# Kernel tuning notes

Measured on AMD Instinct MI355X. Metric: run time of the kernel, lower is better.

Reference implementation:

```python
import jax, jax.numpy as jnp
import numpy as np

B, L, C = 8, 8192, 256
FOCAL_LEVEL = 3
KERNELS = [3, 5, 7]  # focal_factor*k + focal_x[0]
LN_EPS = 1e-3  # keras LayerNormalization default epsilon


def _gelu(x):
    return jax.nn.gelu(x, approximate=False)  # keras 'gelu' is exact


def _layernorm(x, g, b):
    m = jnp.mean(x, axis=-1, keepdims=True)
    v = jnp.var(x, axis=-1, keepdims=True)
    return (x - m) * jax.lax.rsqrt(v + LN_EPS) * g + b


def _conv1d_same(x, w, b):
    # x: [B,L,Cin], w: [K,Cin,Cout]
    y = jax.lax.conv_general_dilated(x, w, window_strides=(1,), padding='SAME',
                                     dimension_numbers=('NWC', 'WIO', 'NWC'))
    return y + b


def setup_inputs() -> dict:
    key = jax.random.key(0)
    ks = jax.random.split(key, 16)
    s = 0.02
    inp = {
        'x': jax.random.normal(ks[0], (B, L, C), dtype=jnp.float32),
        'f_w': jax.random.normal(ks[1], (C, 2 * C + FOCAL_LEVEL + 1), dtype=jnp.float32) * s,
        'f_b': jnp.zeros((2 * C + FOCAL_LEVEL + 1,), dtype=jnp.float32),
        'h_w': jax.random.normal(ks[2], (1, C, C), dtype=jnp.float32) * s,
        'h_b': jnp.zeros((C,), dtype=jnp.float32),
        'proj_w': jax.random.normal(ks[3], (C, C), dtype=jnp.float32) * s,
        'proj_b': jnp.zeros((C,), dtype=jnp.float32),
    }
    for l, K in enumerate(KERNELS):
        inp[f'conv_w{l}'] = jax.random.normal(ks[4 + l], (K, C, C), dtype=jnp.float32) * s
        inp[f'conv_b{l}'] = jnp.zeros((C,), dtype=jnp.float32)
        inp[f'ln_g{l}'] = jnp.ones((C,), dtype=jnp.float32)
        inp[f'ln_b{l}'] = jnp.zeros((C,), dtype=jnp.float32)
    return inp


def reference(x, f_w, f_b,
              conv_w0, conv_b0, ln_g0, ln_b0,
              conv_w1, conv_b1, ln_g1, ln_b1,
              conv_w2, conv_b2, ln_g2, ln_b2,
              h_w, h_b, proj_w, proj_b):
    x_fea = x @ f_w + f_b                      # [B,L,2C+4]
    q = x_fea[..., :C]
    ctx = x_fea[..., C:2 * C]
    gates = x_fea[..., 2 * C:]                 # [B,L,4]

    levels = [(conv_w0, conv_b0, ln_g0, ln_b0),
              (conv_w1, conv_b1, ln_g1, ln_b1),
              (conv_w2, conv_b2, ln_g2, ln_b2)]

    ctx_all = jnp.zeros_like(ctx)
    for l, (cw, cb, lg, lb) in enumerate(levels):
        ctx = _layernorm(_gelu(_conv1d_same(ctx, cw, cb)), lg, lb)
        ctx_all = ctx_all + ctx * gates[..., l:l + 1]

    # global average pool gate (broadcasts over L)
    ctx_global = jnp.mean(ctx, axis=1, keepdims=True) * gates[..., FOCAL_LEVEL:]
    ctx_all = ctx_all + ctx_global

    # h: 1x1 conv == dense
    ctx_all = jnp.einsum('blc,cd->bld', ctx_all, h_w[0]) + h_b
    x_out = (q * ctx_all) @ proj_w + proj_b    # proj_drop is identity at inference
    return x_out
```

## Files before the change

kernel.cpp:

```cpp
#include <hip/hip_runtime.h>
#include <math.h>

#define CDIM 256
#define LSEQ 8192
#define BATCH 8
#define MTOT (BATCH * LSEQ)
#define PADROWS 8208
#define PAD0 8

typedef unsigned short ushort_t;
typedef unsigned int uint_t;

typedef __bf16 bf16x8 __attribute__((ext_vector_type(8)));
typedef float f32x4 __attribute__((ext_vector_type(4)));

__device__ __forceinline__ ushort_t f2bf(float f) {
    union { float f; uint_t u; } v; v.f = f;
    uint_t u = v.u;
    return (ushort_t)((u + 0x7FFFu + ((u >> 16) & 1u)) >> 16);
}
__device__ __forceinline__ float bf2f(ushort_t h) {
    union { uint_t u; float f; } v; v.u = ((uint_t)h) << 16;
    return v.f;
}
__device__ __forceinline__ float gelu_exact(float x) {
    return 0.5f * x * (1.0f + erff(x * 0.70710678118654752440f));
}

__device__ __forceinline__ void gload16(const ushort_t* g, ushort_t* lds) {
    __builtin_amdgcn_global_load_lds(
        reinterpret_cast<__attribute__((address_space(1))) uint_t*>(
            reinterpret_cast<uintptr_t>(g)),
        reinterpret_cast<__attribute__((address_space(3))) uint_t*>(
            reinterpret_cast<uintptr_t>(lds)),
        16, 0, 0);
}

__global__ __launch_bounds__(256) void cvt_f32_bf16(const float* __restrict__ in,
                                                    ushort_t* __restrict__ out) {
    int i = blockIdx.x * 256 + threadIdx.x;
    float4 v = ((const float4*)in)[i];
    ushort4 o = { f2bf(v.x), f2bf(v.y), f2bf(v.z), f2bf(v.w) };
    ((ushort4*)out)[i] = o;
}

__global__ __launch_bounds__(256) void transpose_cvt(const float* __restrict__ in,
                                                     ushort_t* __restrict__ out,
                                                     int K, int N, int ldin, int col0) {
    __shared__ float t[32][33];
    int k0 = blockIdx.x * 32, n0 = blockIdx.y * 32;
    int tx = threadIdx.x, ty = threadIdx.y;
    #pragma unroll
    for (int i = 0; i < 4; i++) {
        int k = k0 + ty + i * 8;
        t[ty + i * 8][tx] = in[(size_t)k * ldin + col0 + n0 + tx];
    }
    __syncthreads();
    #pragma unroll
    for (int i = 0; i < 4; i++) {
        int n = n0 + ty + i * 8;
        out[(size_t)n * K + k0 + tx] = f2bf(t[tx][ty + i * 8]);
    }
}

__global__ __launch_bounds__(256) void zero_guards(ushort_t* __restrict__ ctx_pad) {
    int i = blockIdx.x * 256 + threadIdx.x;
    int c = i & 255;
    int r = (i >> 8) & 15;
    int b = i >> 12;
    int row = b * PADROWS + ((r < 8) ? r : (PADROWS - 16 + r));
    ctx_pad[(size_t)row * CDIM + c] = 0;
}

template <int MODE>
__global__ __launch_bounds__(256) void gemm_bf16(
    const ushort_t* __restrict__ A, const ushort_t* __restrict__ BT,
    const float* __restrict__ bias,
    float* __restrict__ C, ushort_t* __restrict__ q_out, ushort_t* __restrict__ ctx_pad,
    int Ktot)
{
    __shared__ __align__(16) ushort_t As[128 * 32];
    __shared__ __align__(16) ushort_t Bs[128 * 32];
    int tid = threadIdx.x;
    int w = tid >> 6, l = tid & 63;
    int bn = blockIdx.x * 128;
    int by = blockIdx.y;
    long arow0 = (long)by * 128;
    int crow0 = by * 128;

    int wr = w >> 1, wc = w & 1;
    int lr = l & 15, lk = (l >> 4) * 8;
    int sr = l >> 2;
    int sc = (l & 3) * 8;

    f32x4 acc[4][4] = {};

    int nsteps = Ktot >> 5;
    for (int kt = 0; kt < nsteps; ++kt) {
        int k0 = kt << 5;
        #pragma unroll
        for (int jj = 0; jj < 2; ++jj) {
            int j = w * 2 + jj;
            int r = j * 16 + sr;
            gload16(A + (arow0 + r) * CDIM + (k0 + sc), &As[j * 512]);
            gload16(BT + (long)(bn + r) * Ktot + (k0 + sc), &Bs[j * 512]);
        }
        __syncthreads();
        bf16x8 av[4], bv[4];
        #pragma unroll
        for (int m = 0; m < 4; ++m)
            av[m] = *reinterpret_cast<const bf16x8*>(&As[(wr * 64 + m * 16 + lr) * 32 + lk]);
        #pragma unroll
        for (int n = 0; n < 4; ++n)
            bv[n] = *reinterpret_cast<const bf16x8*>(&Bs[(wc * 64 + n * 16 + lr) * 32 + lk]);
        #pragma unroll
        for (int m = 0; m < 4; ++m)
            #pragma unroll
            for (int n = 0; n < 4; ++n)
                acc[m][n] = __builtin_amdgcn_mfma_f32_16x16x32_bf16(av[m], bv[n], acc[m][n], 0, 0, 0);
        __syncthreads();
    }

    int rbase = (l >> 4) * 4;
    #pragma unroll
    for (int n = 0; n < 4; ++n) {
        int col = bn + wc * 64 + n * 16 + lr;
        float bia = bias[col];
        #pragma unroll
        for (int m = 0; m < 4; ++m) {
            int rowb = crow0 + wr * 64 + m * 16 + rbase;
            #pragma unroll
            for (int r = 0; r < 4; ++r) {
                float v = acc[m][n][r] + bia;
                int row = rowb + r;
                if (MODE == 0) {
                    C[(size_t)row * CDIM + col] = v;
                } else if (MODE == 1) {
                    if (col < CDIM) {
                        q_out[(size_t)row * CDIM + col] = f2bf(v);
                    } else {
                        int bb = row >> 13, tb = row & (LSEQ - 1);
                        ctx_pad[((size_t)bb * PADROWS + PAD0 + tb) * CDIM + (col - CDIM)] = f2bf(v);
                    }
                } else {
                    size_t idx = (size_t)row * CDIM + col;
                    q_out[idx] = f2bf(bf2f(q_out[idx]) * v);
                }
            }
        }
    }
}

__device__ __forceinline__ void stageA_chunk(const ushort_t* Arow0, int cc,
                                             ushort_t* asb, int tid, int w) {
    int o = tid;
    int row = o >> 2, cp = o & 3;
    int cg = cp ^ (row & 3);
    gload16(Arow0 + (size_t)row * CDIM + cc * 32 + cg * 8, asb + (size_t)(w * 64) * 8);
    if (tid < 64) {
        int o2 = 512 + tid;
        int row2 = o2 >> 2, cp2 = o2 & 3;
        int cg2 = cp2 ^ (row2 & 3);
        gload16(Arow0 + (size_t)row2 * CDIM + cc * 32 + cg2 * 8, asb + (size_t)512 * 8);
    }
}
__device__ __forceinline__ void stageB_chunk(const ushort_t* BT, int Ktot, int koffB,
                                             ushort_t* bsb, int tid, int w) {
    #pragma unroll
    for (int i = 0; i < 2; ++i) {
        int o = tid + i * 512;
        int n = o >> 2, cp = o & 3;
        int cg = cp ^ ((n >> 1) & 3);
        gload16(BT + (size_t)n * Ktot + koffB + cg * 8, bsb + (size_t)(w * 64 + i * 512) * 8);
    }
}

__global__ __launch_bounds__(512, 4) void conv_fused(
    const ushort_t* __restrict__ A, const ushort_t* __restrict__ BT,
    const float* __restrict__ bias,
    const float* __restrict__ lng, const float* __restrict__ lnb,
    ushort_t* __restrict__ ctx_out, int KW, int Ktot)
{
    __shared__ __align__(16) ushort_t As2[2][144 * 32];
    __shared__ __align__(16) ushort_t Bs[2][256 * 32];

    int tid = threadIdx.x;
    int w = tid >> 6, l = tid & 63;
    int by = blockIdx.x;
    int b = by >> 6;
    int tloc = (by & 63) << 7;
    const ushort_t* Arow0 = A + ((size_t)b * PADROWS + PAD0 + tloc - 8) * CDIM;

    int wr = w >> 2;
    int wc = w & 3;
    int lr = l & 15;
    int quad = l >> 4;

    int P = KW >> 1;
    int hoff = 8 - P;
    f32x4 acc[4][4] = {};

    stageA_chunk(Arow0, 0, As2[0], tid, w);
    stageB_chunk(BT, Ktot, 0, Bs[0], tid, w);
    __syncthreads();

    int nIt = KW * 8;
    int it = 0;
    for (int c = 0; c < 8; ++c) {
        for (int tap = 0; tap < KW; ++tap, ++it) {
            if (tap == 0 && c < 7)
                stageA_chunk(Arow0, c + 1, As2[(c + 1) & 1], tid, w);
            if (it + 1 < nIt) {
                int tapn = tap + 1, cn = c;
                if (tapn == KW) { tapn = 0; cn = c + 1; }
                stageB_chunk(BT, Ktot, tapn * 256 + cn * 32, Bs[(it + 1) & 1], tid, w);
            }
            const ushort_t* asb = As2[c & 1];
            const ushort_t* bsb = Bs[it & 1];
            bf16x8 av[4], bv[4];
            #pragma unroll
            for (int m = 0; m < 4; ++m) {
                int row = wr * 64 + m * 16 + lr + tap + hoff;
                int cs = quad ^ (row & 3);
                av[m] = *reinterpret_cast<const bf16x8*>(&asb[row * 32 + cs * 8]);
            }
            #pragma unroll
            for (int n = 0; n < 4; ++n) {
                int nn = wc * 64 + n * 16 + lr;
                int cs = quad ^ ((nn >> 1) & 3);
                bv[n] = *reinterpret_cast<const bf16x8*>(&bsb[nn * 32 + cs * 8]);
            }
            #pragma unroll
            for (int m = 0; m < 4; ++m)
                #pragma unroll
                for (int n = 0; n < 4; ++n)
                    acc[m][n] = __builtin_amdgcn_mfma_f32_16x16x32_bf16(av[m], bv[n], acc[m][n], 0, 0, 0);
            __syncthreads();
        }
    }

    float* rs = (float*)&Bs[0][0];
    float* rq = rs + 512;
    float bias_c[4], lng_c[4], lnb_c[4];
    #pragma unroll
    for (int n = 0; n < 4; ++n) {
        int col = wc * 64 + n * 16 + lr;
        bias_c[n] = bias[col];
        lng_c[n] = lng[col];
        lnb_c[n] = lnb[col];
    }
    #pragma unroll
    for (int m = 0; m < 4; ++m) {
        #pragma unroll
        for (int r = 0; r < 4; ++r) {
            float s = 0.0f, sq = 0.0f;
            #pragma unroll
            for (int n = 0; n < 4; ++n) {
                float v = acc[m][n][r] + bias_c[n];
                v = gelu_exact(v);
                acc[m][n][r] = v;
                s += v; sq += v * v;
            }
            s += __shfl_xor(s, 1);  sq += __shfl_xor(sq, 1);
            s += __shfl_xor(s, 2);  sq += __shfl_xor(sq, 2);
            s += __shfl_xor(s, 4);  sq += __shfl_xor(sq, 4);
            s += __shfl_xor(s, 8);  sq += __shfl_xor(sq, 8);
            if (lr == 0) {
                int rl = wr * 64 + m * 16 + quad * 4 + r;
                rs[rl * 4 + wc] = s;
                rq[rl * 4 + wc] = sq;
            }
        }
    }
    __syncthreads();
    #pragma unroll
    for (int m = 0; m < 4; ++m) {
        #pragma unroll
        for (int r = 0; r < 4; ++r) {
            int rl = wr * 64 + m * 16 + quad * 4 + r;
            float mean = (rs[rl * 4] + rs[rl * 4 + 1] + rs[rl * 4 + 2] + rs[rl * 4 + 3]) * (1.0f / 256.0f);
            float var = (rq[rl * 4] + rq[rl * 4 + 1] + rq[rl * 4 + 2] + rq[rl * 4 + 3]) * (1.0f / 256.0f) - mean * mean;
            float inv = rsqrtf(var + 1e-3f);
            int trow = tloc + rl;
            ushort_t* cp = ctx_out + ((size_t)b * PADROWS + PAD0 + trow) * CDIM;
            #pragma unroll
            for (int n = 0; n < 4; ++n) {
                int col = wc * 64 + n * 16 + lr;
                float y = (acc[m][n][r] - mean) * inv * lng_c[n] + lnb_c[n];
                cp[col] = f2bf(y);
            }
        }
    }
}

__global__ __launch_bounds__(256) void gates_kernel(const float* __restrict__ x,
                                                    const float* __restrict__ f_w,
                                                    const float* __restrict__ f_b,
                                                    float* __restrict__ gates) {
    __shared__ float fcol[256][4];
    int tid = threadIdx.x;
    #pragma unroll
    for (int j = 0; j < 4; ++j) fcol[tid][j] = f_w[(size_t)tid * 516 + 512 + j];
    __syncthreads();
    int w = tid >> 6, l = tid & 63;
    int t = blockIdx.x * 4 + w;
    float4 xv = ((const float4*)(x + (size_t)t * CDIM))[l];
    int c = l * 4;
    float a[4];
    #pragma unroll
    for (int j = 0; j < 4; ++j)
        a[j] = xv.x * fcol[c][j] + xv.y * fcol[c + 1][j] + xv.z * fcol[c + 2][j] + xv.w * fcol[c + 3][j];
    #pragma unroll
    for (int off = 32; off >= 1; off >>= 1)
        #pragma unroll
        for (int j = 0; j < 4; ++j) a[j] += __shfl_xor(a[j], off);
    if (l == 0) {
        #pragma unroll
        for (int j = 0; j < 4; ++j) gates[(size_t)t * 4 + j] = a[j] + f_b[512 + j];
    }
}

__global__ __launch_bounds__(256) void col_mean_partial(const ushort_t* __restrict__ ctx_pad,
                                                        float* __restrict__ partial) {
    int b = blockIdx.x, chunk = blockIdx.y, c = threadIdx.x;
    const ushort_t* base = ctx_pad + ((size_t)b * PADROWS + PAD0 + chunk * 256) * CDIM + c;
    float s = 0.0f;
    for (int r = 0; r < 256; ++r) s += bf2f(base[(size_t)r * CDIM]);
    partial[((size_t)b * 32 + chunk) * CDIM + c] = s;
}

__global__ __launch_bounds__(256) void col_mean_final(const float* __restrict__ partial,
                                                      float* __restrict__ meanv) {
    int b = blockIdx.x, c = threadIdx.x;
    float s = 0.0f;
    for (int i = 0; i < 32; ++i) s += partial[((size_t)b * 32 + i) * CDIM + c];
    meanv[b * CDIM + c] = s * (1.0f / (float)LSEQ);
}

__global__ __launch_bounds__(256) void finalize_A(
    const ushort_t* __restrict__ c0buf, const ushort_t* __restrict__ c1buf,
    const ushort_t* __restrict__ c2buf,
    const float* __restrict__ meanv, const float* __restrict__ gates,
    ushort_t* __restrict__ A_bf)
{
    int i = blockIdx.x * 256 + threadIdx.x;
    int t = i >> 5;
    int c8 = (i & 31) * 8;
    int b = t >> 13, tb = t & (LSEQ - 1);
    size_t pidx = ((size_t)b * PADROWS + PAD0 + tb) * CDIM + c8;
    const float* g = gates + (size_t)t * 4;
    float g0 = g[0], g1 = g[1], g2 = g[2], g3 = g[3];
    ushort4 a0 = *(const ushort4*)(c0buf + pidx);
    ushort4 a1 = *(const ushort4*)(c0buf + pidx + 4);
    ushort4 b0 = *(const ushort4*)(c1buf + pidx);
    ushort4 b1 = *(const ushort4*)(c1buf + pidx + 4);
    ushort4 d0 = *(const ushort4*)(c2buf + pidx);
    ushort4 d1 = *(const ushort4*)(c2buf + pidx + 4);
    const float* mv = meanv + b * CDIM + c8;
    ushort_t out[8];
    ushort_t va[8] = { a0.x, a0.y, a0.z, a0.w, a1.x, a1.y, a1.z, a1.w };
    ushort_t vb[8] = { b0.x, b0.y, b0.z, b0.w, b1.x, b1.y, b1.z, b1.w };
    ushort_t vd[8] = { d0.x, d0.y, d0.z, d0.w, d1.x, d1.y, d1.z, d1.w };
    #pragma unroll
    for (int j = 0; j < 8; ++j) {
        float v = bf2f(va[j]) * g0 + bf2f(vb[j]) * g1 + bf2f(vd[j]) * g2 + mv[j] * g3;
        out[j] = f2bf(v);
    }
    *(ushort4*)(A_bf + (size_t)t * CDIM + c8)     = make_ushort4(out[0], out[1], out[2], out[3]);
    *(ushort4*)(A_bf + (size_t)t * CDIM + c8 + 4) = make_ushort4(out[4], out[5], out[6], out[7]);
}

extern "C" void kernel_launch(void* const* d_in, const int* in_sizes, int n_in,
                              void* d_out, int out_size, void* d_ws, size_t ws_size,
                              hipStream_t stream) {
    const float* x      = (const float*)d_in[0];
    const float* f_w    = (const float*)d_in[1];
    const float* f_b    = (const float*)d_in[2];
    const float* h_w    = (const float*)d_in[3];
    const float* h_b    = (const float*)d_in[4];
    const float* proj_w = (const float*)d_in[5];
    const float* proj_b = (const float*)d_in[6];
    const float* conv_w[3] = { (const float*)d_in[7],  (const float*)d_in[11], (const float*)d_in[15] };
    const float* conv_b[3] = { (const float*)d_in[8],  (const float*)d_in[12], (const float*)d_in[16] };
    const float* ln_g[3]   = { (const float*)d_in[9],  (const float*)d_in[13], (const float*)d_in[17] };
    const float* ln_b[3]   = { (const float*)d_in[10], (const float*)d_in[14], (const float*)d_in[18] };

    const size_t MC = (size_t)MTOT * CDIM;
    const size_t PADC = (size_t)BATCH * PADROWS * CDIM;
    char* w = (char*)d_ws;
    ushort_t* x_bf  = (ushort_t*)w;  w += MC * 2;
    ushort_t* q_bf  = (ushort_t*)w;  w += MC * 2;
    ushort_t* ctxF  = (ushort_t*)w;  w += PADC * 2;
    ushort_t* ctx0  = (ushort_t*)w;  w += PADC * 2;
    ushort_t* ctx1  = (ushort_t*)w;  w += PADC * 2;
    ushort_t* ctx2  = (ushort_t*)w;  w += PADC * 2;
    float* gates    = (float*)w;     w += (size_t)MTOT * 4 * 4;
    float* partial  = (float*)w;     w += (size_t)8 * 32 * CDIM * 4;
    float* meanv    = (float*)w;     w += (size_t)8 * CDIM * 4;
    ushort_t* f_wT  = (ushort_t*)w;  w += (size_t)512 * 256 * 2;
    ushort_t* convT0 = (ushort_t*)w; w += (size_t)768 * 256 * 2;
    ushort_t* convT1 = (ushort_t*)w; w += (size_t)1280 * 256 * 2;
    ushort_t* convT2 = (ushort_t*)w; w += (size_t)1792 * 256 * 2;
    ushort_t* h_wT   = (ushort_t*)w; w += (size_t)256 * 256 * 2;
    ushort_t* proj_wT = (ushort_t*)w; w += (size_t)256 * 256 * 2;
    ushort_t* A_bf = x_bf;

    dim3 blk(256);
    dim3 t8(32, 8);

    cvt_f32_bf16<<<dim3(MC / 4 / 256), blk, 0, stream>>>(x, x_bf);
    transpose_cvt<<<dim3(8, 16), t8, 0, stream>>>(f_w, f_wT, 256, 512, 516, 0);
    transpose_cvt<<<dim3(24, 8), t8, 0, stream>>>(conv_w[0], convT0, 768, 256, 256, 0);
    transpose_cvt<<<dim3(40, 8), t8, 0, stream>>>(conv_w[1], convT1, 1280, 256, 256, 0);
    transpose_cvt<<<dim3(56, 8), t8, 0, stream>>>(conv_w[2], convT2, 1792, 256, 256, 0);
    transpose_cvt<<<dim3(8, 8), t8, 0, stream>>>(h_w, h_wT, 256, 256, 256, 0);
    transpose_cvt<<<dim3(8, 8), t8, 0, stream>>>(proj_w, proj_wT, 256, 256, 256, 0);
    zero_guards<<<dim3(128), blk, 0, stream>>>(ctxF);
    zero_guards<<<dim3(128), blk, 0, stream>>>(ctx0);
    zero_guards<<<dim3(128), blk, 0, stream>>>(ctx1);
    zero_guards<<<dim3(128), blk, 0, stream>>>(ctx2);

    gemm_bf16<1><<<dim3(4, 512), blk, 0, stream>>>(x_bf, f_wT, f_b,
        nullptr, q_bf, ctxF, 256);
    gates_kernel<<<dim3(MTOT / 4), blk, 0, stream>>>(x, f_w, f_b, gates);

    conv_fused<<<dim3(512), dim3(512), 0, stream>>>(ctxF, convT0, conv_b[0],
        ln_g[0], ln_b[0], ctx0, 3, 768);
    conv_fused<<<dim3(512), dim3(512), 0, stream>>>(ctx0, convT1, conv_b[1],
        ln_g[1], ln_b[1], ctx1, 5, 1280);
    conv_fused<<<dim3(512), dim3(512), 0, stream>>>(ctx1, convT2, conv_b[2],
        ln_g[2], ln_b[2], ctx2, 7, 1792);

    col_mean_partial<<<dim3(BATCH, 32), blk, 0, stream>>>(ctx2, partial);
    col_mean_final<<<dim3(BATCH), blk, 0, stream>>>(partial, meanv);

    finalize_A<<<dim3(MTOT * 32 / 256), blk, 0, stream>>>(ctx0, ctx1, ctx2,
        meanv, gates, A_bf);

    gemm_bf16<2><<<dim3(2, 512), blk, 0, stream>>>(A_bf, h_wT, h_b,
        nullptr, q_bf, nullptr, 256);
    gemm_bf16<0><<<dim3(2, 512), blk, 0, stream>>>(q_bf, proj_wT, proj_b,
        (float*)d_out, nullptr, nullptr, 256);
}
```

Before: 376.9 us.

## Triple-buffer conv staging with prefetch distance two and counted vmcnt waits

The fused conv GEMM loop moves from double to triple buffering for both the activation (A) and weight (B) LDS tiles, so loads are issued two iterations ahead. The full __syncthreads is replaced by an s_waitcnt on vmcnt with a per-iteration count plus a raw s_barrier, so newer loads can stay in flight across the barrier. The A-tile LDS swizzle changes to match the B-tile pattern. The extra buffers raise LDS use per block, which can cut the number of resident blocks per CU. The hand-counted waits are easy to get wrong.

```diff
diff --git a/kernel.cpp b/kernel.cpp
--- a/kernel.cpp
+++ b/kernel.cpp
@@ -34,6 +34,15 @@
         reinterpret_cast<__attribute__((address_space(3))) uint_t*>(
             reinterpret_cast<uintptr_t>(lds)),
         16, 0, 0);
+}
+
+__device__ __forceinline__ void wait_bar(int n) {
+    if (n == 0)      asm volatile("s_waitcnt vmcnt(0) lgkmcnt(0)" ::: "memory");
+    else if (n == 2) asm volatile("s_waitcnt vmcnt(2) lgkmcnt(0)" ::: "memory");
+    else if (n == 3) asm volatile("s_waitcnt vmcnt(3) lgkmcnt(0)" ::: "memory");
+    else             asm volatile("s_waitcnt vmcnt(4) lgkmcnt(0)" ::: "memory");
+    __builtin_amdgcn_s_barrier();
+    __builtin_amdgcn_sched_barrier(0);
 }
 
 __global__ __launch_bounds__(256) void cvt_f32_bf16(const float* __restrict__ in,
@@ -151,27 +160,27 @@
     }
 }
 
-__device__ __forceinline__ void stageA_chunk(const ushort_t* Arow0, int cc,
-                                             ushort_t* asb, int tid, int w) {
-    int o = tid;
-    int row = o >> 2, cp = o & 3;
-    int cg = cp ^ (row & 3);
+__device__ __forceinline__ void stageA128(const ushort_t* Arow0, int cc,
+                                          ushort_t* asb, int tid, int w) {
+    int row = tid >> 2, cp = tid & 3;
+    int cg = cp ^ ((row >> 1) & 3);
     gload16(Arow0 + (size_t)row * CDIM + cc * 32 + cg * 8, asb + (size_t)(w * 64) * 8);
     if (tid < 64) {
         int o2 = 512 + tid;
         int row2 = o2 >> 2, cp2 = o2 & 3;
-        int cg2 = cp2 ^ (row2 & 3);
+        int cg2 = cp2 ^ ((row2 >> 1) & 3);
         gload16(Arow0 + (size_t)row2 * CDIM + cc * 32 + cg2 * 8, asb + (size_t)512 * 8);
     }
 }
-__device__ __forceinline__ void stageB_chunk(const ushort_t* BT, int Ktot, int koffB,
-                                             ushort_t* bsb, int tid, int w) {
+__device__ __forceinline__ void stageB128(const ushort_t* BT, int Ktot, int koffB,
+                                          ushort_t* bsb, int tid) {
     #pragma unroll
     for (int i = 0; i < 2; ++i) {
         int o = tid + i * 512;
         int n = o >> 2, cp = o & 3;
         int cg = cp ^ ((n >> 1) & 3);
-        gload16(BT + (size_t)n * Ktot + koffB + cg * 8, bsb + (size_t)(w * 64 + i * 512) * 8);
+        gload16(BT + (size_t)n * Ktot + koffB + cg * 8,
+                bsb + (size_t)((o >> 6) * 64) * 8);
     }
 }
 
@@ -181,8 +190,8 @@
     const float* __restrict__ lng, const float* __restrict__ lnb,
     ushort_t* __restrict__ ctx_out, int KW, int Ktot)
 {
-    __shared__ __align__(16) ushort_t As2[2][144 * 32];
-    __shared__ __align__(16) ushort_t Bs[2][256 * 32];
+    __shared__ __align__(16) ushort_t As3[3][144 * 32];
+    __shared__ __align__(16) ushort_t Bs[3][256 * 32];
 
     int tid = threadIdx.x;
     int w = tid >> 6, l = tid & 63;
@@ -200,28 +209,37 @@
     int hoff = 8 - P;
     f32x4 acc[4][4] = {};
 
-    stageA_chunk(Arow0, 0, As2[0], tid, w);
-    stageB_chunk(BT, Ktot, 0, Bs[0], tid, w);
-    __syncthreads();
+    stageA128(Arow0, 0, As3[0], tid, w);
+    stageA128(Arow0, 1, As3[1], tid, w);
+    stageB128(BT, Ktot, 0, Bs[0], tid);
+    stageB128(BT, Ktot, 1 * 256, Bs[1], tid);
+    asm volatile("s_waitcnt vmcnt(0)" ::: "memory");
+    __builtin_amdgcn_s_barrier();
+    __builtin_amdgcn_sched_barrier(0);
 
     int nIt = KW * 8;
     int it = 0;
+    int acur = 0;
+    int bcur = 0;
+    int tap2 = 2, c2 = 0;
     for (int c = 0; c < 8; ++c) {
         for (int tap = 0; tap < KW; ++tap, ++it) {
-            if (tap == 0 && c < 7)
-                stageA_chunk(Arow0, c + 1, As2[(c + 1) & 1], tid, w);
-            if (it + 1 < nIt) {
-                int tapn = tap + 1, cn = c;
-                if (tapn == KW) { tapn = 0; cn = c + 1; }
-                stageB_chunk(BT, Ktot, tapn * 256 + cn * 32, Bs[(it + 1) & 1], tid, w);
-            }
-            const ushort_t* asb = As2[c & 1];
-            const ushort_t* bsb = Bs[it & 1];
+            if (it + 2 < nIt) {
+                int bstg = bcur + 2; if (bstg >= 3) bstg -= 3;
+                stageB128(BT, Ktot, tap2 * 256 + c2 * 32, Bs[bstg], tid);
+            }
+            if (tap == 0 && c <= 5) {
+                int astg = acur + 2; if (astg >= 3) astg -= 3;
+                stageA128(Arow0, c + 2, As3[astg], tid, w);
+            }
+
+            const ushort_t* asb = As3[acur];
+            const ushort_t* bsb = Bs[bcur];
             bf16x8 av[4], bv[4];
             #pragma unroll
             for (int m = 0; m < 4; ++m) {
                 int row = wr * 64 + m * 16 + lr + tap + hoff;
-                int cs = quad ^ (row & 3);
+                int cs = quad ^ ((row >> 1) & 3);
                 av[m] = *reinterpret_cast<const bf16x8*>(&asb[row * 32 + cs * 8]);
             }
             #pragma unroll
@@ -235,11 +253,20 @@
                 #pragma unroll
                 for (int n = 0; n < 4; ++n)
                     acc[m][n] = __builtin_amdgcn_mfma_f32_16x16x32_bf16(av[m], bv[n], acc[m][n], 0, 0, 0);
-            __syncthreads();
+
+            int wn;
+            if (it + 2 >= nIt)               wn = 0;
+            else if (tap <= 1 && c <= 5)     wn = (w == 0) ? 4 : 3;
+            else                             wn = 2;
+            wait_bar(wn);
+
+            bcur = bcur + 1; if (bcur == 3) bcur = 0;
+            tap2 = tap2 + 1; if (tap2 == KW) { tap2 = 0; c2 = c2 + 1; }
         }
-    }
-
-    float* rs = (float*)&Bs[0][0];
+        acur = acur + 1; if (acur == 3) acur = 0;
+    }
+
+    float* rs = (float*)&As3[0][0];
     float* rq = rs + 512;
     float bias_c[4], lng_c[4], lnb_c[4];
     #pragma unroll
```

Result: slower. 384.5 us (+2.0%).
